# Optimization experiments

Hardware: AMD Instinct MI355X
Metric: run time of the kernel (lower is better)

Reference implementation:

```python
import jax, jax.numpy as jnp
import numpy as np

N = 800_000      # total nodes across the batch
D = 128          # feature width (neurons = [128, 128, 128])
G = 4096         # number of graphs (segments)


def setup_inputs() -> dict:
    key = jax.random.key(0)
    ks = jax.random.split(key, 10)
    s = 1.0 / np.sqrt(D)
    features = jax.random.normal(ks[0], (N, D), dtype=jnp.float32)
    batch_index = jnp.sort(jax.random.randint(ks[1], (N,), 0, G, dtype=jnp.int64))
    # feature_mlp: Linear(D->D) + SiLU, Linear(D->D)
    Wf1 = jax.random.normal(ks[2], (D, D), dtype=jnp.float32) * s
    bf1 = jnp.zeros((D,), dtype=jnp.float32)
    Wf2 = jax.random.normal(ks[3], (D, D), dtype=jnp.float32) * s
    bf2 = jnp.zeros((D,), dtype=jnp.float32)
    # weight_mlp: Linear(D->D) + SiLU, Linear(D->1)
    Ww1 = jax.random.normal(ks[4], (D, D), dtype=jnp.float32) * s
    bw1 = jnp.zeros((D,), dtype=jnp.float32)
    Ww2 = jax.random.normal(ks[5], (D, 1), dtype=jnp.float32) * s
    bw2 = jnp.zeros((1,), dtype=jnp.float32)
    return {
        "features": features, "batch_index": batch_index,
        "Wf1": Wf1, "bf1": bf1, "Wf2": Wf2, "bf2": bf2,
        "Ww1": Ww1, "bw1": bw1, "Ww2": Ww2, "bw2": bw2,
    }


def reference(features, batch_index, Wf1, bf1, Wf2, bf2, Ww1, bw1, Ww2, bw2):
    silu = jax.nn.silu
    # feature MLP: SiLU on hidden layer, linear output
    pf = silu(features @ Wf1 + bf1) @ Wf2 + bf2          # [N, D]
    # weight MLP -> per-node scalar logit
    w = silu(features @ Ww1 + bw1) @ Ww2 + bw2           # [N, 1]
    seg = batch_index
    # unsorted segment softmax over each graph's nodes
    maxes = jax.ops.segment_max(w, seg, num_segments=G)  # [G, 1]
    w_exp = jnp.exp(w - maxes[seg])                      # [N, 1]
    w_sum = jax.ops.segment_sum(w_exp, seg, num_segments=G)
    soft_w = w_exp / (w_sum[seg] + 1e-16)                # [N, 1]
    # weighted sum-pool per graph
    return jax.ops.segment_sum(pf * soft_w, seg, num_segments=G)  # [G, D]
```

## Files before the change

kernel.cpp:

```cpp
#include <hip/hip_runtime.h>

typedef unsigned short ushort_t;
typedef unsigned short ushort8 __attribute__((ext_vector_type(8)));
typedef unsigned short ushort4v __attribute__((ext_vector_type(4)));
typedef __bf16 bf16x8 __attribute__((ext_vector_type(8)));
typedef float f32x4 __attribute__((ext_vector_type(4)));

__device__ __forceinline__ unsigned short f2bf(float f){
  union { float f; unsigned int u; } v; v.f = f;
  unsigned int u = v.u;
  u += 0x7fffu + ((u >> 16) & 1u);
  return (unsigned short)(u >> 16);
}
__device__ __forceinline__ float bf2f(unsigned short b){
  union { float f; unsigned int u; } v; v.u = ((unsigned int)b) << 16;
  return v.f;
}
__device__ __forceinline__ float fsilu(float x){
  return x * __builtin_amdgcn_rcpf(1.0f + __expf(-x));
}

__global__ void k0_prep(const float* __restrict__ Wf1, const float* __restrict__ Wf2,
                        const float* __restrict__ Ww1, ushort_t* __restrict__ wt)
{
  int idx = blockIdx.x * 256 + threadIdx.x;
  int mtx = idx >> 14, rem = idx & 16383;
  int n = rem >> 7, k = rem & 127;
  const float* src = (mtx == 0) ? Ww1 : (mtx == 1) ? Wf1 : Wf2;
  wt[idx] = f2bf(src[k*128 + n]);
}

__global__ __launch_bounds__(256, 2)
void k1_mlp(const float* __restrict__ X, const ushort_t* __restrict__ Wt,
            const float* __restrict__ bf1, const float* __restrict__ bf2,
            const float* __restrict__ bw1, const float* __restrict__ ww2,
            const float* __restrict__ bw2,
            ushort_t* __restrict__ pf, float* __restrict__ wout)
{
  __shared__ ushort_t Xs[128*128];
  __shared__ ushort_t Ws[128*128];
  const int tid = threadIdx.x;
  const int lane = tid & 63;
  const int wv = tid >> 6;
  const int cbase = lane & 15;
  const int kq = lane >> 4;
  const long r0 = (long)blockIdx.x * 128;
  const int wrow0 = wv * 32;

  float vbw1[8], vbf1[8], vbf2[8], vww2[8];
#pragma unroll
  for (int f = 0; f < 8; f++){
    vbw1[f] = bw1[f*16+cbase];
    vbf1[f] = bf1[f*16+cbase];
    vbf2[f] = bf2[f*16+cbase];
    vww2[f] = ww2[f*16+cbase];
  }
  const float sbw2 = bw2[0];

#pragma unroll
  for (int it = 0; it < 16; it++){
    int idx = it*256 + tid;
    int row = idx >> 5, c4 = idx & 31;
    const float4 v = *(const float4*)(X + (r0+row)*128 + c4*4);
    ushort4v h;
    h[0]=f2bf(v.x); h[1]=f2bf(v.y); h[2]=f2bf(v.z); h[3]=f2bf(v.w);
    *(ushort4v*)(Xs + row*128 + ((((c4>>1) ^ (row&7))<<3)) + ((c4&1)<<2)) = h;
  }

  auto stage_w = [&](const ushort_t* src){
#pragma unroll
    for (int it = 0; it < 8; it++){
      int idx = it*256 + tid;
      int row = idx >> 4, ch = idx & 15;
      ushort8 v = *(const ushort8*)(src + row*128 + ch*8);
      *(ushort8*)(Ws + row*128 + ((ch ^ (row&7))<<3)) = v;
    }
  };

  f32x4 acc[2][8];
  auto zero_acc = [&]{
#pragma unroll
    for (int a=0;a<2;a++)
#pragma unroll
      for (int b=0;b<8;b++) acc[a][b] = (f32x4){0.f,0.f,0.f,0.f};
  };
  auto gemm = [&]{
#pragma unroll
    for (int ks = 0; ks < 4; ks++){
      bf16x8 av[2], bv[8];
#pragma unroll
      for (int fm = 0; fm < 2; fm++){
        int row = wrow0 + fm*16 + cbase;
        av[fm] = __builtin_bit_cast(bf16x8,
          *(const ushort8*)(Xs + row*128 + (((ks*4+kq) ^ (row&7))<<3)));
      }
#pragma unroll
      for (int fn = 0; fn < 8; fn++){
        int col = fn*16 + cbase;
        bv[fn] = __builtin_bit_cast(bf16x8,
          *(const ushort8*)(Ws + col*128 + (((ks*4+kq) ^ (col&7))<<3)));
      }
#pragma unroll
      for (int fm = 0; fm < 2; fm++)
#pragma unroll
        for (int fn = 0; fn < 8; fn++)
          acc[fm][fn] = __builtin_amdgcn_mfma_f32_16x16x32_bf16(
                          av[fm], bv[fn], acc[fm][fn], 0, 0, 0);
    }
  };

  stage_w(Wt + 0);
  __syncthreads();
  zero_acc(); gemm();
#pragma unroll
  for (int fm = 0; fm < 2; fm++){
#pragma unroll
    for (int reg = 0; reg < 4; reg++){
      float p = 0.f;
#pragma unroll
      for (int fn = 0; fn < 8; fn++)
        p += fsilu(acc[fm][fn][reg] + vbw1[fn]) * vww2[fn];
      p += __shfl_xor(p, 1); p += __shfl_xor(p, 2);
      p += __shfl_xor(p, 4); p += __shfl_xor(p, 8);
      if (cbase == 0)
        wout[r0 + wrow0 + fm*16 + kq*4 + reg] = p + sbw2;
    }
  }
  __syncthreads();

  stage_w(Wt + 16384);
  __syncthreads();
  zero_acc(); gemm();
#pragma unroll
  for (int fm=0;fm<2;fm++)
#pragma unroll
    for (int fn=0;fn<8;fn++)
#pragma unroll
      for (int reg=0;reg<4;reg++){
        int row = wrow0 + fm*16 + kq*4 + reg;
        int col = fn*16 + cbase;
        float h = fsilu(acc[fm][fn][reg] + vbf1[fn]);
        Xs[row*128 + ((((col>>3) ^ (row&7))<<3)) + (col&7)] = f2bf(h);
      }
  __syncthreads();

  stage_w(Wt + 32768);
  __syncthreads();
  zero_acc(); gemm();
#pragma unroll
  for (int fm=0;fm<2;fm++)
#pragma unroll
    for (int fn=0;fn<8;fn++)
#pragma unroll
      for (int reg=0;reg<4;reg++){
        int row = wrow0 + fm*16 + kq*4 + reg;
        int col = fn*16 + cbase;
        Xs[row*128 + ((((col>>3) ^ (row&7))<<3)) + (col&7)]
          = f2bf(acc[fm][fn][reg] + vbf2[fn]);
      }
  __syncthreads();
#pragma unroll
  for (int j = 0; j < 8; j++){
    int flat = j*64 + lane;
    int rsl = flat >> 4, ch = flat & 15;
    int row = wrow0 + rsl;
    ushort8 v = *(const ushort8*)(Xs + row*128 + ((ch ^ (row&7))<<3));
    *(ushort8*)(pf + (r0+row)*128 + ch*8) = v;
  }
}

__device__ __forceinline__ int lbound(const int* __restrict__ a, int n, int v){
  int lo = 0, hi = n;
  while (lo < hi){
    int mid = (lo + hi) >> 1;
    if (a[mid] < v) lo = mid + 1; else hi = mid;
  }
  return lo;
}

__global__ __launch_bounds__(256)
void k2_pool(const float* __restrict__ w, const ushort_t* __restrict__ pf,
             const int* __restrict__ seg, float* __restrict__ out, int Nn)
{
  __shared__ int sse[2];
  __shared__ float sred[512];
  const int tid = threadIdx.x;
  const int g = blockIdx.x;
  if (tid < 2) sse[tid] = lbound(seg, Nn, g + tid);
  __syncthreads();
  const int s = sse[0], e = sse[1];

  float m = -3.0e38f;
  for (int i = s + tid; i < e; i += 256) m = fmaxf(m, w[i]);
#pragma unroll
  for (int d = 32; d; d >>= 1) m = fmaxf(m, __shfl_xor(m, d));
  if ((tid & 63) == 0) sred[tid >> 6] = m;
  __syncthreads();
  m = fmaxf(fmaxf(sred[0], sred[1]), fmaxf(sred[2], sred[3]));
  __syncthreads();

  float ssum = 0.f;
  for (int i = s + tid; i < e; i += 256) ssum += __expf(w[i] - m);
#pragma unroll
  for (int d = 32; d; d >>= 1) ssum += __shfl_xor(ssum, d);
  if ((tid & 63) == 0) sred[tid >> 6] = ssum;
  __syncthreads();
  const float invS = 1.0f / (sred[0] + sred[1] + sred[2] + sred[3] + 1e-16f);
  __syncthreads();

  float a0 = 0.f, a1 = 0.f;
  const int sub = tid >> 6, pr = tid & 63;
  for (int i = s + sub; i < e; i += 4){
    const float en = __expf(w[i] - m) * invS;
    const unsigned int u = *(const unsigned int*)(pf + (size_t)i*128 + pr*2);
    a0 += en * bf2f((unsigned short)(u & 0xffffu));
    a1 += en * bf2f((unsigned short)(u >> 16));
  }
  sred[tid*2] = a0; sred[tid*2+1] = a1;
  __syncthreads();
  if (tid < 64){
    float r0a = 0.f, r1a = 0.f;
#pragma unroll
    for (int q = 0; q < 4; q++){
      r0a += sred[(q*64+tid)*2];
      r1a += sred[(q*64+tid)*2+1];
    }
    out[(size_t)g*128 + tid*2]     = r0a;
    out[(size_t)g*128 + tid*2 + 1] = r1a;
  }
}

extern "C" void kernel_launch(void* const* d_in, const int* in_sizes, int n_in,
                              void* d_out, int out_size, void* d_ws, size_t ws_size,
                              hipStream_t stream) {
  const float* X   = (const float*)d_in[0];
  const int*   seg = (const int*)d_in[1];
  const float* Wf1 = (const float*)d_in[2];
  const float* bf1 = (const float*)d_in[3];
  const float* Wf2 = (const float*)d_in[4];
  const float* bf2 = (const float*)d_in[5];
  const float* Ww1 = (const float*)d_in[6];
  const float* bw1 = (const float*)d_in[7];
  const float* Ww2 = (const float*)d_in[8];
  const float* bw2 = (const float*)d_in[9];
  float* out = (float*)d_out;

  const int Nn = in_sizes[0] / 128;
  const int G  = out_size / 128;

  ushort_t* pf   = (ushort_t*)d_ws;
  float*    wbuf = (float*)((char*)d_ws + (size_t)Nn*128*2);
  ushort_t* wt   = (ushort_t*)((char*)d_ws + (size_t)Nn*128*2 + (size_t)Nn*4);

  k0_prep<<<192, 256, 0, stream>>>(Wf1, Wf2, Ww1, wt);
  k1_mlp<<<Nn/128, 256, 0, stream>>>(X, wt, bf1, bf2, bw1, Ww2, bw2, pf, wbuf);
  k2_pool<<<G, 256, 0, stream>>>(wbuf, pf, seg, out, Nn);
}
```

Measured before the change: 709.4 us.

## Make MLP kernel persistent with resident weights and per-wave register-prefetched tiles

The MLP kernel now launches a fixed grid of 256 blocks of 8 waves that keep all three bf16 weight matrices resident in 96 KB of LDS. Each wave loops over 16-row chunks, prefetching the next chunk's fp32 inputs into registers while it runs the three GEMMs on the current chunk in a private LDS slab, with no block-level barriers. This is meant to remove the repeated per-block weight staging and barrier stalls and to overlap global loads with MFMA work. The pooling kernel also switches to 16-byte vector loads of pf with shuffle reductions. The costs are large LDS use (128 KB per block, so likely one block per CU) and MFMA tiles only 16 rows tall, which lowers weight reuse per LDS read.

```diff
diff --git a/kernel.cpp b/kernel.cpp
--- a/kernel.cpp
+++ b/kernel.cpp
@@ -19,6 +19,11 @@
 __device__ __forceinline__ float fsilu(float x){
   return x * __builtin_amdgcn_rcpf(1.0f + __expf(-x));
 }
+
+#define GRID1   256
+#define WAVES1  8
+#define THR1    (WAVES1*64)
+#define GWAVES  (GRID1*WAVES1)
 
 __global__ void k0_prep(const float* __restrict__ Wf1, const float* __restrict__ Wf2,
                         const float* __restrict__ Ww1, ushort_t* __restrict__ wt)
@@ -30,22 +35,25 @@
   wt[idx] = f2bf(src[k*128 + n]);
 }
 
-__global__ __launch_bounds__(256, 2)
+__global__ __launch_bounds__(THR1, 2)
 void k1_mlp(const float* __restrict__ X, const ushort_t* __restrict__ Wt,
             const float* __restrict__ bf1, const float* __restrict__ bf2,
             const float* __restrict__ bw1, const float* __restrict__ ww2,
             const float* __restrict__ bw2,
-            ushort_t* __restrict__ pf, float* __restrict__ wout)
+            ushort_t* __restrict__ pf, float* __restrict__ wout, int C)
 {
-  __shared__ ushort_t Xs[128*128];
-  __shared__ ushort_t Ws[128*128];
-  const int tid = threadIdx.x;
-  const int lane = tid & 63;
-  const int wv = tid >> 6;
+  __shared__ ushort_t lds[65536];
+  const int tid   = threadIdx.x;
+  const int lane  = tid & 63;
+  const int wv    = tid >> 6;
   const int cbase = lane & 15;
-  const int kq = lane >> 4;
-  const long r0 = (long)blockIdx.x * 128;
-  const int wrow0 = wv * 32;
+  const int kq    = lane >> 4;
+
+  for (int i = tid; i < 6144; i += THR1){
+    int mrow = i >> 4, ch = i & 15;
+    ushort8 v = *(const ushort8*)(Wt + mrow*128 + ch*8);
+    *(ushort8*)(lds + mrow*128 + ((ch ^ (mrow & 7)) << 3)) = v;
+  }
 
   float vbw1[8], vbf1[8], vbf2[8], vww2[8];
 #pragma unroll
@@ -57,115 +65,103 @@
   }
   const float sbw2 = bw2[0];
 
-#pragma unroll
-  for (int it = 0; it < 16; it++){
-    int idx = it*256 + tid;
-    int row = idx >> 5, c4 = idx & 31;
-    const float4 v = *(const float4*)(X + (r0+row)*128 + c4*4);
-    ushort4v h;
-    h[0]=f2bf(v.x); h[1]=f2bf(v.y); h[2]=f2bf(v.z); h[3]=f2bf(v.w);
-    *(ushort4v*)(Xs + row*128 + ((((c4>>1) ^ (row&7))<<3)) + ((c4&1)<<2)) = h;
-  }
-
-  auto stage_w = [&](const ushort_t* src){
+  __syncthreads();
+
+  ushort_t* slab = lds + 49152 + wv*2048;
+
+  float4 xr[8];
+  auto load_xr = [&](long c){
 #pragma unroll
     for (int it = 0; it < 8; it++){
-      int idx = it*256 + tid;
-      int row = idx >> 4, ch = idx & 15;
-      ushort8 v = *(const ushort8*)(src + row*128 + ch*8);
-      *(ushort8*)(Ws + row*128 + ((ch ^ (row&7))<<3)) = v;
+      int idx = it*64 + lane;
+      int row = idx >> 5, c4 = idx & 31;
+      xr[it] = *(const float4*)(X + (c*16 + row)*128 + c4*4);
     }
   };
 
-  f32x4 acc[2][8];
-  auto zero_acc = [&]{
-#pragma unroll
-    for (int a=0;a<2;a++)
-#pragma unroll
-      for (int b=0;b<8;b++) acc[a][b] = (f32x4){0.f,0.f,0.f,0.f};
-  };
-  auto gemm = [&]{
+  f32x4 acc[8];
+  auto gemmv = [&](int mtx){
+#pragma unroll
+    for (int i = 0; i < 8; i++) acc[i] = (f32x4){0.f,0.f,0.f,0.f};
 #pragma unroll
     for (int ks = 0; ks < 4; ks++){
-      bf16x8 av[2], bv[8];
-#pragma unroll
-      for (int fm = 0; fm < 2; fm++){
-        int row = wrow0 + fm*16 + cbase;
-        av[fm] = __builtin_bit_cast(bf16x8,
-          *(const ushort8*)(Xs + row*128 + (((ks*4+kq) ^ (row&7))<<3)));
-      }
+      const int chunkid = ks*4 + kq;
+      const int arow = cbase;
+      bf16x8 av = __builtin_bit_cast(bf16x8,
+        *(const ushort8*)(slab + arow*128 + ((chunkid ^ (arow & 7)) << 3)));
 #pragma unroll
       for (int fn = 0; fn < 8; fn++){
         int col = fn*16 + cbase;
-        bv[fn] = __builtin_bit_cast(bf16x8,
-          *(const ushort8*)(Ws + col*128 + (((ks*4+kq) ^ (col&7))<<3)));
-      }
-#pragma unroll
-      for (int fm = 0; fm < 2; fm++)
+        bf16x8 bv = __builtin_bit_cast(bf16x8,
+          *(const ushort8*)(lds + mtx*16384 + col*128 + ((chunkid ^ (col & 7)) << 3)));
+        acc[fn] = __builtin_amdgcn_mfma_f32_16x16x32_bf16(av, bv, acc[fn], 0, 0, 0);
+      }
+    }
+  };
+
+  const int gw = blockIdx.x * WAVES1 + wv;
+  long c = gw;
+  if (c < C) load_xr(c);
+  for (; c < C; c += GWAVES){
+#pragma unroll
+    for (int it = 0; it < 8; it++){
+      int idx = it*64 + lane;
+      int row = idx >> 5, c4 = idx & 31;
+      ushort4v h;
+      h[0]=f2bf(xr[it].x); h[1]=f2bf(xr[it].y);
+      h[2]=f2bf(xr[it].z); h[3]=f2bf(xr[it].w);
+      *(ushort4v*)(slab + row*128 + (((c4>>1) ^ (row&7)) << 3) + ((c4&1) << 2)) = h;
+    }
+    long cn = c + GWAVES;
+    if (cn < C) load_xr(cn);
+
+    gemmv(0);
+    {
+      f32x4 pr;
+#pragma unroll
+      for (int reg = 0; reg < 4; reg++){
+        float p = 0.f;
 #pragma unroll
         for (int fn = 0; fn < 8; fn++)
-          acc[fm][fn] = __builtin_amdgcn_mfma_f32_16x16x32_bf16(
-                          av[fm], bv[fn], acc[fm][fn], 0, 0, 0);
-    }
-  };
-
-  stage_w(Wt + 0);
-  __syncthreads();
-  zero_acc(); gemm();
-#pragma unroll
-  for (int fm = 0; fm < 2; fm++){
-#pragma unroll
-    for (int reg = 0; reg < 4; reg++){
-      float p = 0.f;
-#pragma unroll
-      for (int fn = 0; fn < 8; fn++)
-        p += fsilu(acc[fm][fn][reg] + vbw1[fn]) * vww2[fn];
-      p += __shfl_xor(p, 1); p += __shfl_xor(p, 2);
-      p += __shfl_xor(p, 4); p += __shfl_xor(p, 8);
+          p += fsilu(acc[fn][reg] + vbw1[fn]) * vww2[fn];
+        pr[reg] = p;
+      }
+#pragma unroll
+      for (int reg = 0; reg < 4; reg++){
+        pr[reg] += __shfl_xor(pr[reg], 1); pr[reg] += __shfl_xor(pr[reg], 2);
+        pr[reg] += __shfl_xor(pr[reg], 4); pr[reg] += __shfl_xor(pr[reg], 8);
+        pr[reg] += sbw2;
+      }
       if (cbase == 0)
-        wout[r0 + wrow0 + fm*16 + kq*4 + reg] = p + sbw2;
-    }
-  }
-  __syncthreads();
-
-  stage_w(Wt + 16384);
-  __syncthreads();
-  zero_acc(); gemm();
-#pragma unroll
-  for (int fm=0;fm<2;fm++)
-#pragma unroll
-    for (int fn=0;fn<8;fn++)
-#pragma unroll
-      for (int reg=0;reg<4;reg++){
-        int row = wrow0 + fm*16 + kq*4 + reg;
-        int col = fn*16 + cbase;
-        float h = fsilu(acc[fm][fn][reg] + vbf1[fn]);
-        Xs[row*128 + ((((col>>3) ^ (row&7))<<3)) + (col&7)] = f2bf(h);
-      }
-  __syncthreads();
-
-  stage_w(Wt + 32768);
-  __syncthreads();
-  zero_acc(); gemm();
-#pragma unroll
-  for (int fm=0;fm<2;fm++)
-#pragma unroll
-    for (int fn=0;fn<8;fn++)
-#pragma unroll
-      for (int reg=0;reg<4;reg++){
-        int row = wrow0 + fm*16 + kq*4 + reg;
-        int col = fn*16 + cbase;
-        Xs[row*128 + ((((col>>3) ^ (row&7))<<3)) + (col&7)]
-          = f2bf(acc[fm][fn][reg] + vbf2[fn]);
-      }
-  __syncthreads();
-#pragma unroll
-  for (int j = 0; j < 8; j++){
-    int flat = j*64 + lane;
-    int rsl = flat >> 4, ch = flat & 15;
-    int row = wrow0 + rsl;
-    ushort8 v = *(const ushort8*)(Xs + row*128 + ((ch ^ (row&7))<<3));
-    *(ushort8*)(pf + (r0+row)*128 + ch*8) = v;
+        *(float4*)(wout + c*16 + kq*4) = (float4){pr[0], pr[1], pr[2], pr[3]};
+    }
+
+    gemmv(1);
+#pragma unroll
+    for (int fn = 0; fn < 8; fn++)
+#pragma unroll
+      for (int reg = 0; reg < 4; reg++){
+        int row = kq*4 + reg, col = fn*16 + cbase;
+        slab[row*128 + ((((col>>3) ^ (row&7)) << 3)) + (col&7)]
+          = f2bf(fsilu(acc[fn][reg] + vbf1[fn]));
+      }
+
+    gemmv(2);
+#pragma unroll
+    for (int fn = 0; fn < 8; fn++)
+#pragma unroll
+      for (int reg = 0; reg < 4; reg++){
+        int row = kq*4 + reg, col = fn*16 + cbase;
+        slab[row*128 + ((((col>>3) ^ (row&7)) << 3)) + (col&7)]
+          = f2bf(acc[fn][reg] + vbf2[fn]);
+      }
+#pragma unroll
+    for (int j = 0; j < 4; j++){
+      int flat = j*64 + lane;
+      int row = flat >> 4, ch = flat & 15;
+      ushort8 v = *(const ushort8*)(slab + row*128 + ((ch ^ (row&7)) << 3));
+      *(ushort8*)(pf + (c*16 + row)*128 + ch*8) = v;
+    }
   }
 }
 
@@ -183,9 +179,13 @@
              const int* __restrict__ seg, float* __restrict__ out, int Nn)
 {
   __shared__ int sse[2];
-  __shared__ float sred[512];
-  const int tid = threadIdx.x;
-  const int g = blockIdx.x;
+  __shared__ float sred[4*128];
+  const int tid  = threadIdx.x;
+  const int g    = blockIdx.x;
+  const int wv   = tid >> 6;
+  const int lane = tid & 63;
+  const int q    = lane >> 4;
+  const int cb   = lane & 15;
   if (tid < 2) sse[tid] = lbound(seg, Nn, g + tid);
   __syncthreads();
   const int s = sse[0], e = sse[1];
@@ -194,7 +194,7 @@
   for (int i = s + tid; i < e; i += 256) m = fmaxf(m, w[i]);
 #pragma unroll
   for (int d = 32; d; d >>= 1) m = fmaxf(m, __shfl_xor(m, d));
-  if ((tid & 63) == 0) sred[tid >> 6] = m;
+  if (lane == 0) sred[wv] = m;
   __syncthreads();
   m = fmaxf(fmaxf(sred[0], sred[1]), fmaxf(sred[2], sred[3]));
   __syncthreads();
@@ -203,30 +203,33 @@
   for (int i = s + tid; i < e; i += 256) ssum += __expf(w[i] - m);
 #pragma unroll
   for (int d = 32; d; d >>= 1) ssum += __shfl_xor(ssum, d);
-  if ((tid & 63) == 0) sred[tid >> 6] = ssum;
+  if (lane == 0) sred[wv] = ssum;
   __syncthreads();
   const float invS = 1.0f / (sred[0] + sred[1] + sred[2] + sred[3] + 1e-16f);
   __syncthreads();
 
-  float a0 = 0.f, a1 = 0.f;
-  const int sub = tid >> 6, pr = tid & 63;
-  for (int i = s + sub; i < e; i += 4){
+  float a[8];
+#pragma unroll
+  for (int j = 0; j < 8; j++) a[j] = 0.f;
+  for (int i = s + wv*4 + q; i < e; i += 16){
     const float en = __expf(w[i] - m) * invS;
-    const unsigned int u = *(const unsigned int*)(pf + (size_t)i*128 + pr*2);
-    a0 += en * bf2f((unsigned short)(u & 0xffffu));
-    a1 += en * bf2f((unsigned short)(u >> 16));
-  }
-  sred[tid*2] = a0; sred[tid*2+1] = a1;
-  __syncthreads();
-  if (tid < 64){
-    float r0a = 0.f, r1a = 0.f;
-#pragma unroll
-    for (int q = 0; q < 4; q++){
-      r0a += sred[(q*64+tid)*2];
-      r1a += sred[(q*64+tid)*2+1];
-    }
-    out[(size_t)g*128 + tid*2]     = r0a;
-    out[(size_t)g*128 + tid*2 + 1] = r1a;
+    ushort8 v = *(const ushort8*)(pf + (size_t)i*128 + cb*8);
+#pragma unroll
+    for (int j = 0; j < 8; j++) a[j] += en * bf2f(v[j]);
+  }
+#pragma unroll
+  for (int j = 0; j < 8; j++){
+    a[j] += __shfl_xor(a[j], 16);
+    a[j] += __shfl_xor(a[j], 32);
+  }
+  if (lane < 16){
+#pragma unroll
+    for (int j = 0; j < 8; j++) sred[wv*128 + cb*8 + j] = a[j];
+  }
+  __syncthreads();
+  if (tid < 128){
+    out[(size_t)g*128 + tid]
+      = sred[tid] + sred[128 + tid] + sred[256 + tid] + sred[384 + tid];
   }
 }
 
@@ -247,12 +250,13 @@
 
   const int Nn = in_sizes[0] / 128;
   const int G  = out_size / 128;
+  const int C  = Nn / 16;
 
   ushort_t* pf   = (ushort_t*)d_ws;
   float*    wbuf = (float*)((char*)d_ws + (size_t)Nn*128*2);
   ushort_t* wt   = (ushort_t*)((char*)d_ws + (size_t)Nn*128*2 + (size_t)Nn*4);
 
   k0_prep<<<192, 256, 0, stream>>>(Wf1, Wf2, Ww1, wt);
-  k1_mlp<<<Nn/128, 256, 0, stream>>>(X, wt, bf1, bf2, bw1, Ww2, bw2, pf, wbuf);
+  k1_mlp<<<GRID1, THR1, 0, stream>>>(X, wt, bf1, bf2, bw1, Ww2, bw2, pf, wbuf, C);
   k2_pool<<<G, 256, 0, stream>>>(wbuf, pf, seg, out, Nn);
 }
```

New measurement: 668.6 us. 5.8% less time.
